# Kernel optimization log

Measured on AMD Instinct MI355X. Metric: run time of the kernel, lower is better.

## Reference

```python
import jax, jax.numpy as jnp
import numpy as np

L = 20        # num layers (TTS LM)
Q = 512       # query length
PAST = 512    # past_kv_len
END = PAST + Q  # end_step = 1024
MAXS = 2048   # max_seq_len
D = 896       # hidden size
NKV = 2       # KV heads
NQ = 14       # Q heads
G = NQ // NKV # GQA repeat = 7
HD = 64       # head dim
FF = 4864     # SwiGLU intermediate (Qwen2.5-0.5B)
EPS = 1e-6
SCALE = 1.0 / np.sqrt(HD)


def rms_norm(x, w):
    return x * jax.lax.rsqrt(jnp.mean(x * x, axis=-1, keepdims=True) + EPS) * w


def rotate_half(x):
    x1, x2 = jnp.split(x, 2, axis=-1)
    return jnp.concatenate([-x2, x1], axis=-1)


def setup_inputs() -> dict:
    key = jax.random.key(0)
    ks = jax.random.split(key, 24)
    s = 0.02
    inp = {
        'hidden_states': jax.random.normal(ks[0], (1, Q, D), jnp.float32),
        'position_cos': jax.random.uniform(ks[1], (1, Q, HD), jnp.float32, -1.0, 1.0),
        'position_sin': jax.random.uniform(ks[2], (1, Q, HD), jnp.float32, -1.0, 1.0),
        'attention_mask': jnp.zeros((1, 1, Q, END), jnp.float32),
        'inject_mode': jnp.zeros((1,), jnp.float32),
        'inject_k': jax.random.normal(ks[3], (1, L * NKV, Q, HD), jnp.float32),
        'inject_v': jax.random.normal(ks[4], (1, L * NKV, Q, HD), jnp.float32),
        'k_cache': (jax.random.normal(ks[5], (L, 1, NKV, MAXS, HD), jnp.float32) * 0.5).astype(jnp.float16),
        'v_cache': (jax.random.normal(ks[6], (L, 1, NKV, MAXS, HD), jnp.float32) * 0.5).astype(jnp.float16),
        'Wq': jax.random.normal(ks[7], (L, D, NQ * HD), jnp.float32) * s,
        'bq': jax.random.normal(ks[8], (L, NQ * HD), jnp.float32) * s,
        'Wk': jax.random.normal(ks[9], (L, D, NKV * HD), jnp.float32) * s,
        'bk': jax.random.normal(ks[10], (L, NKV * HD), jnp.float32) * s,
        'Wv': jax.random.normal(ks[11], (L, D, NKV * HD), jnp.float32) * s,
        'bv': jax.random.normal(ks[12], (L, NKV * HD), jnp.float32) * s,
        'Wo': jax.random.normal(ks[13], (L, NQ * HD, D), jnp.float32) * s,
        'ln1': jnp.ones((L, D), jnp.float32),
        'ln2': jnp.ones((L, D), jnp.float32),
        'Wg': jax.random.normal(ks[14], (L, D, FF), jnp.float32) * s,
        'Wu': jax.random.normal(ks[15], (L, D, FF), jnp.float32) * s,
        'Wd': jax.random.normal(ks[16], (L, FF, D), jnp.float32) * s,
        'final_w': jnp.ones((D,), jnp.float32),
    }
    return inp


def reference(hidden_states, position_cos, position_sin, attention_mask,
              inject_mode, inject_k, inject_v, k_cache, v_cache,
              Wq, bq, Wk, bk, Wv, bv, Wo, ln1, ln2, Wg, Wu, Wd, final_w):
    cos = position_cos[:, None]   # [1,1,Q,HD]
    sin = position_sin[:, None]
    inj = inject_mode[0]
    normal = 1.0 - inj
    mask = attention_mask[:, None]  # [1,1,1,Q,END] broadcast over (g,h)
    # per-layer inject slices: [L,1,NKV,Q,HD]
    ik = jnp.transpose(inject_k.reshape(1, L, NKV, Q, HD), (1, 0, 2, 3, 4))
    iv = jnp.transpose(inject_v.reshape(1, L, NKV, Q, HD), (1, 0, 2, 3, 4))

    def layer_fn(h, p):
        (wq, bq_, wk, bk_, wv, bv_, wo, l1, l2, wg, wu, wd, kc, vc, ikl, ivl) = p
        residual = h
        x = rms_norm(h, l1)
        q = (x @ wq + bq_).reshape(1, Q, NQ, HD).transpose(0, 2, 1, 3)   # [1,NQ,Q,HD]
        k = (x @ wk + bk_).reshape(1, Q, NKV, HD).transpose(0, 2, 1, 3)  # [1,NKV,Q,HD]
        v = (x @ wv + bv_).reshape(1, Q, NKV, HD).transpose(0, 2, 1, 3)
        q = q * cos + rotate_half(q) * sin
        k = k * cos + rotate_half(k) * sin
        k = normal * k + inj * ikl
        v = normal * v + inj * ivl
        kc = kc.at[:, :, PAST:END].set(k.astype(jnp.float16))
        vc = vc.at[:, :, PAST:END].set(v.astype(jnp.float16))
        kf = kc[:, :, :END].astype(jnp.float32)  # [1,NKV,END,HD]
        vf = vc[:, :, :END].astype(jnp.float32)
        qg = q.reshape(1, NKV, G, Q, HD)         # grouped GQA (== repeat_kv)
        scores = jnp.einsum('bghqd,bgkd->bghqk', qg, kf) * SCALE + mask
        w = jax.nn.softmax(scores, axis=-1)
        o = jnp.einsum('bghqk,bgkd->bghqd', w, vf)
        o = o.reshape(1, NQ, Q, HD).transpose(0, 2, 1, 3).reshape(1, Q, NQ * HD)
        h = residual + o @ wo
        residual = h
        x = rms_norm(h, l2)
        h = residual + (jax.nn.silu(x @ wg) * (x @ wu)) @ wd
        return h, None

    xs = (Wq, bq, Wk, bk, Wv, bv, Wo, ln1, ln2, Wg, Wu, Wd, k_cache, v_cache, ik, iv)
    h, _ = jax.lax.scan(layer_fn, hidden_states, xs)
    return rms_norm(h, final_w)
```

## Files before the change

kernel.cpp:

```cpp
#include <hip/hip_runtime.h>
#include <hip/hip_fp16.h>
#include <hip/hip_cooperative_groups.h>

namespace cg = cooperative_groups;

#define NLAYER 20
#define QLEN 512
#define PAST 512
#define ENDS 1024
#define MAXS 2048
#define DMODEL 896
#define NKV 2
#define NQ 14
#define GQ 7
#define HD 64
#define FF 4864
#define RMSEPS 1e-6f
#define ATT_SCALE 0.125f

typedef _Float16 f16x8 __attribute__((ext_vector_type(8)));
typedef float f32x4 __attribute__((ext_vector_type(4)));
typedef unsigned int u32_;

__device__ __forceinline__ void gld16(const void* g, void* l) {
    __builtin_amdgcn_global_load_lds(
        (const __attribute__((address_space(1))) u32_*)g,
        (__attribute__((address_space(3))) u32_*)l, 16, 0, 0);
}

union SmemU {
    struct { __half As[16384]; __half Bs[16384]; } g;
    struct { __half S[16512]; float rowinv[16]; } a;
    __half Tp[128 * 130];
    struct { float red[4]; } r;
};

#define GEMM_STAGE64(A_, lda_, B_, ldb_, Kps_)                                  \
    const int lane = t & 63, wave = t >> 6;                                     \
    const int wm = wave >> 1, wn = wave & 1;                                    \
    const int m0 = by * 128, n0 = bx * 128;                                     \
    const int kb0 = bz * (Kps_);                                                \
    const int la = lane & 15, kg = lane >> 4;                                   \
    const int nIter = (Kps_) >> 6;                                              \
    const int srow = t >> 3;                                                    \
    const int gsw = ((t & 7) ^ (srow & 7)) * 8;                                 \
    f32x4 acc[4][4] = {};                                                       \
    {                                                                           \
        _Pragma("unroll")                                                       \
        for (int q = 0; q < 4; q++) {                                           \
            gld16(&(A_)[(size_t)(m0 + q * 32 + srow) * (lda_) + kb0 + gsw], &As[q * 2048 + t * 8]); \
            gld16(&(B_)[(size_t)(n0 + q * 32 + srow) * (ldb_) + kb0 + gsw], &Bs[q * 2048 + t * 8]); \
        }                                                                       \
    }                                                                           \
    int buf = 0;                                                                \
    for (int kt = 0; kt < nIter; kt++) {                                        \
        __syncthreads();                                                        \
        if (kt + 1 < nIter) {                                                   \
            const int ko = kb0 + (kt + 1) * 64;                                 \
            const int lb = (buf ^ 1) * 8192;                                    \
            _Pragma("unroll")                                                   \
            for (int q = 0; q < 4; q++) {                                       \
                gld16(&(A_)[(size_t)(m0 + q * 32 + srow) * (lda_) + ko + gsw], &As[lb + q * 2048 + t * 8]); \
                gld16(&(B_)[(size_t)(n0 + q * 32 + srow) * (ldb_) + ko + gsw], &Bs[lb + q * 2048 + t * 8]); \
            }                                                                   \
        }                                                                       \
        _Pragma("unroll")                                                       \
        for (int kk = 0; kk < 2; kk++) {                                        \
            f16x8 av[4], bv[4];                                                 \
            const int g = kk * 4 + kg;                                          \
            _Pragma("unroll")                                                   \
            for (int i = 0; i < 4; i++) {                                       \
                const int R = wm * 64 + i * 16 + la;                            \
                av[i] = *(const f16x8*)&As[buf * 8192 + R * 64 + ((g ^ (R & 7)) * 8)]; \
            }                                                                   \
            _Pragma("unroll")                                                   \
            for (int j = 0; j < 4; j++) {                                       \
                const int R = wn * 64 + j * 16 + la;                            \
                bv[j] = *(const f16x8*)&Bs[buf * 8192 + R * 64 + ((g ^ (R & 7)) * 8)]; \
            }                                                                   \
            _Pragma("unroll")                                                   \
            for (int i = 0; i < 4; i++)                                         \
                _Pragma("unroll")                                               \
                for (int j = 0; j < 4; j++)                                     \
                    acc[i][j] = __builtin_amdgcn_mfma_f32_16x16x32_f16(av[i], bv[j], acc[i][j], 0, 0, 0); \
        }                                                                       \
        buf ^= 1;                                                               \
    }                                                                           \
    __syncthreads();

__device__ __forceinline__ void gemm_body(
    const __half* __restrict__ A, int lda, const __half* __restrict__ B, int ldb,
    float* __restrict__ outP, __half* __restrict__ actP, int N, int Kps, int mode,
    int bx, int by, int bz, int t, __half* As, __half* Bs)
{
    GEMM_STAGE64(A, lda, B, ldb, Kps)
    const int r0 = m0 + wm * 64 + kg * 4;
    const int c0 = n0 + wn * 64 + la;
    if (mode == 0) {
        float* o = outP + (size_t)bz * QLEN * N;
#pragma unroll
        for (int i = 0; i < 4; i++)
#pragma unroll
            for (int j = 0; j < 4; j++)
#pragma unroll
                for (int r = 0; r < 4; r++)
                    o[(size_t)(r0 + i * 16 + r) * N + c0 + j * 16] = acc[i][j][r];
    } else {
#pragma unroll
        for (int i = 0; i < 4; i++)
#pragma unroll
            for (int j = 0; j < 4; j++)
#pragma unroll
                for (int r = 0; r < 4; r++) {
                    float v = acc[i][j][r];
                    float other = __shfl_xor(v, 1);
                    if (!(la & 1)) {
                        const int c = c0 + j * 16;
                        const int row = r0 + i * 16 + r;
                        float sg = v / (1.f + __expf(-v));
                        actP[(size_t)row * FF + (c >> 1)] = __float2half(sg * other);
                    }
                }
    }
}

__device__ __forceinline__ void gemm_qkv_body(
    const __half* __restrict__ A, const __half* __restrict__ B,
    const float* __restrict__ bqkv, const float* __restrict__ cosb,
    const float* __restrict__ sinb, float inj,
    const float* __restrict__ injk, const float* __restrict__ injv,
    __half* __restrict__ qr, __half* __restrict__ Ka, __half* __restrict__ Vt,
    int layer, int bx, int by, int t, __half* As, __half* Bs)
{
    const int bz = 0;
    GEMM_STAGE64(A, DMODEL, B, DMODEL, 896)
    const int r0 = m0 + wm * 64 + kg * 4;
    const int c0 = n0 + wn * 64 + la;
    const float nrm = 1.f - inj;
#pragma unroll
    for (int i = 0; i < 4; i++)
#pragma unroll
        for (int j = 0; j < 4; j++)
#pragma unroll
            for (int r = 0; r < 4; r++) {
                const int pn = r0 + i * 16 + r;
                const int c = c0 + j * 16;
                const int d = c & 63;
                float v = acc[i][j][r] + bqkv[c];
                if (c < 1024) {
                    float pvv = acc[i][j ^ 2][r] + bqkv[c ^ 32];
                    float rot = (d < 32) ? -pvv : pvv;
                    float rv = v * cosb[pn * HD + d] + rot * sinb[pn * HD + d];
                    if (c < 896) {
                        qr[((size_t)(c >> 6) * QLEN + pn) * HD + d] = __float2half(rv);
                    } else {
                        const int kvh = (c - 896) >> 6;
                        float kn = nrm * rv + inj * injk[(((size_t)layer * NKV + kvh) * QLEN + pn) * HD + d];
                        Ka[((size_t)kvh * ENDS + PAST + pn) * HD + d] = __float2half(kn);
                    }
                } else {
                    const int kvh = (c - 1024) >> 6;
                    float vn = nrm * v + inj * injv[(((size_t)layer * NKV + kvh) * QLEN + pn) * HD + d];
                    Vt[((size_t)kvh * HD + d) * ENDS + PAST + pn] = __float2half(vn);
                }
            }
}

__device__ __forceinline__ void prep_body(
    const float* __restrict__ Wq, const float* __restrict__ Wk, const float* __restrict__ Wv,
    const float* __restrict__ Wo, const float* __restrict__ Wg, const float* __restrict__ Wu,
    const float* __restrict__ Wd, int layer, int z, int bx, int t, __half* Tp,
    __half* __restrict__ dstW)
{
    const int K = (z == 3) ? FF : DMODEL;
    const int N = (z == 0) ? 1152 : (z == 2) ? 2 * FF : DMODEL;
    const int tilesN = N / 128;
    const int tk = bx / tilesN, tn = bx % tilesN;
    const int k0 = tk * 128, n0 = tn * 128;
    const float* src; int ldn, nc0; int isU = 0;
    if (z == 0) {
        if (n0 < 896)        { src = Wq + (size_t)layer * 896 * 896; ldn = 896; nc0 = n0; }
        else if (n0 < 1024)  { src = Wk + (size_t)layer * 896 * 128; ldn = 128; nc0 = n0 - 896; }
        else                 { src = Wv + (size_t)layer * 896 * 128; ldn = 128; nc0 = n0 - 1024; }
    } else if (z == 1) { src = Wo + (size_t)layer * 896 * 896; ldn = 896; nc0 = n0; }
    else if (z == 2) {
        if (n0 < FF) { src = Wg + (size_t)layer * 896 * FF; ldn = FF; nc0 = n0; }
        else         { src = Wu + (size_t)layer * 896 * FF; ldn = FF; nc0 = n0 - FF; isU = 1; }
    } else { src = Wd + (size_t)layer * FF * 896; ldn = 896; nc0 = n0; }

    __syncthreads();
    const int r8 = t >> 5, cc = (t & 31) * 4;
#pragma unroll
    for (int half = 0; half < 2; half++) {
        float4 v[8];
#pragma unroll
        for (int q = 0; q < 8; q++) {
            const int row = half * 64 + q * 8 + r8;
            v[q] = *(const float4*)&src[(size_t)(k0 + row) * ldn + nc0 + cc];
        }
#pragma unroll
        for (int q = 0; q < 8; q++) {
            const int row = half * 64 + q * 8 + r8;
            __half2 p0 = __halves2half2(__float2half_rn(v[q].x), __float2half_rn(v[q].y));
            __half2 p1 = __halves2half2(__float2half_rn(v[q].z), __float2half_rn(v[q].w));
            *(__half2*)&Tp[row * 130 + cc] = p0;
            *(__half2*)&Tp[row * 130 + cc + 2] = p1;
        }
    }
    __syncthreads();
    {
        const int nr = t >> 1, kh = (t & 1) * 64;
        const int drow = (z == 2) ? (2 * (nc0 + nr) + isU) : (n0 + nr);
        __half tmp[64];
#pragma unroll
        for (int kk = 0; kk < 64; kk++)
            tmp[kk] = Tp[(kh + kk) * 130 + nr];
        __half* dst = dstW + (size_t)drow * K + k0 + kh;
#pragma unroll
        for (int q = 0; q < 8; q++)
            *(uint4*)(dst + q * 8) = *(const uint4*)&tmp[q * 8];
    }
    __syncthreads();
}

__device__ __forceinline__ void prep_dispatch(
    const float* Wq, const float* Wk, const float* Wv, const float* Wo,
    const float* Wg, const float* Wu, const float* Wd,
    const float* bq, const float* bk, const float* bv,
    int layer, int j, int t, __half* Tp,
    __half* wq, __half* wo, __half* wgu, __half* wd, float* bqkv)
{
    int z; __half* dst; int bx = j;
    if (j < 63)         { z = 0; dst = wq; }
    else if (j < 112)   { z = 1; dst = wo;  bx -= 63; }
    else if (j < 644)   { z = 2; dst = wgu; bx -= 112; }
    else                { z = 3; dst = wd;  bx -= 644; }
    prep_body(Wq, Wk, Wv, Wo, Wg, Wu, Wd, layer, z, bx, t, Tp, dst);
    if (z == 0 && bx == 0) {
        for (int i = t; i < 1152; i += 256) {
            float b = (i < 896) ? bq[(size_t)layer * 896 + i]
                    : (i < 1024) ? bk[(size_t)layer * 128 + i - 896]
                                 : bv[(size_t)layer * 128 + i - 1024];
            bqkv[i] = b;
        }
    }
}

__device__ __forceinline__ void cache_copy_body(
    const float* __restrict__ kc32, const float* __restrict__ vc32, int layer,
    __half* __restrict__ Ka, __half* __restrict__ Vt, int p, int lt)
{
    const int kvh = lt >> 6, d = lt & 63;
    const size_t idx = (((size_t)layer * NKV + kvh) * MAXS + p) * HD + d;
    Ka[((size_t)kvh * ENDS + p) * HD + d] = __float2half(kc32[idx]);
    Vt[((size_t)kvh * HD + d) * ENDS + p] = __float2half(vc32[idx]);
}

__device__ __forceinline__ void ropekv_body(
    const float* __restrict__ part, const float* __restrict__ bias,
    const float* __restrict__ cosb, const float* __restrict__ sinb,
    const float* __restrict__ injm, const float* __restrict__ injk,
    const float* __restrict__ injv, const float* __restrict__ kc32,
    const float* __restrict__ vc32, int layer, int nsplit,
    __half* __restrict__ qr, __half* __restrict__ Ka, __half* __restrict__ Vt,
    int p, int lt)
{
    const int kvh = lt >> 6, d = lt & 63;
    if (p < PAST) { cache_copy_body(kc32, vc32, layer, Ka, Vt, p, lt); return; }
    const int pn = p - PAST;
    const float inj = injm[0], nrm = 1.f - inj;
    const float* rb = part + (size_t)pn * 1152;
    const size_t sst = (size_t)QLEN * 1152;
    auto rsum = [&](int c) {
        float x = bias[c];
        for (int s = 0; s < nsplit; s++) x += rb[(size_t)s * sst + c];
        return x;
    };
    for (int idx = lt; idx < NQ * HD; idx += 128) {
        const int dd = idx & 63;
        float x = rsum(idx);
        int pc = (dd < 32) ? idx + 32 : idx - 32;
        float pv = rsum(pc);
        if (dd < 32) pv = -pv;
        float rv = x * cosb[pn * HD + dd] + pv * sinb[pn * HD + dd];
        qr[((size_t)(idx >> 6) * QLEN + pn) * HD + dd] = __float2half(rv);
    }
    {
        const int c = NQ * HD + lt;
        float x = rsum(c);
        int pc = (d < 32) ? c + 32 : c - 32;
        float pv = rsum(pc);
        if (d < 32) pv = -pv;
        float rv = x * cosb[pn * HD + d] + pv * sinb[pn * HD + d];
        float kn = nrm * rv + inj * injk[(((size_t)layer * NKV + kvh) * QLEN + pn) * HD + d];
        Ka[((size_t)kvh * ENDS + PAST + pn) * HD + d] = __float2half(kn);
        const int cv = NQ * HD + NKV * HD + lt;
        float vv = rsum(cv);
        float vn = nrm * vv + inj * injv[(((size_t)layer * NKV + kvh) * QLEN + pn) * HD + d];
        Vt[((size_t)kvh * HD + d) * ENDS + PAST + pn] = __float2half(vn);
    }
}

__device__ __forceinline__ int sswz(int row, int col) {
    return row * 1032 + (col ^ ((row & 7) << 3));
}

__device__ __forceinline__ void attn_body(
    const __half* __restrict__ qr, const __half* __restrict__ Ka,
    const __half* __restrict__ Vt, const float* __restrict__ mask,
    __half* __restrict__ ob, int q0, int h, int t, __half* S, float* rowinv)
{
    const int kv = h / GQ;
    const int lane = t & 63, w = t >> 6;
    const int la = lane & 15, kg = lane >> 4;

    const f16x8* qp = (const f16x8*)&qr[((size_t)h * QLEN + q0 + la) * HD + kg * 8];
    const f16x8 qa0 = qp[0], qa1 = qp[4];
    __syncthreads();

    for (int kb = 0; kb < 256; kb += 16) {
        const int key = w * 256 + kb + la;
        const f16x8* kp = (const f16x8*)&Ka[((size_t)kv * ENDS + key) * HD + kg * 8];
        f32x4 s4 = {0.f, 0.f, 0.f, 0.f};
        s4 = __builtin_amdgcn_mfma_f32_16x16x32_f16(qa0, kp[0], s4, 0, 0, 0);
        s4 = __builtin_amdgcn_mfma_f32_16x16x32_f16(qa1, kp[4], s4, 0, 0, 0);
#pragma unroll
        for (int r = 0; r < 4; r++) {
            const int row = kg * 4 + r;
            float sv = s4[r] * ATT_SCALE + mask[(size_t)(q0 + row) * ENDS + key];
            S[sswz(row, key)] = __float2half(sv);
        }
    }
    __syncthreads();
    {
        const int row = w * 4 + kg;
        float mx = -1e30f;
        for (int j = 0; j < 64; j++)
            mx = fmaxf(mx, __half2float(S[sswz(row, la + 16 * j)]));
        for (int o = 1; o < 16; o <<= 1) mx = fmaxf(mx, __shfl_xor(mx, o));
        float sum = 0.f;
        for (int j = 0; j < 64; j++) {
            const int idx = sswz(row, la + 16 * j);
            float e = __expf(__half2float(S[idx]) - mx);
            S[idx] = __float2half(e);
            sum += e;
        }
        for (int o = 1; o < 16; o <<= 1) sum += __shfl_xor(sum, o);
        if (la == 0) rowinv[row] = 1.f / sum;
    }
    __syncthreads();
    {
        const int d = 16 * w + la;
        const __half* vrow = &Vt[((size_t)kv * HD + d) * ENDS];
        f32x4 acc = {0.f, 0.f, 0.f, 0.f};
        for (int ks = 0; ks < ENDS; ks += 32) {
            f16x8 pa = *(const f16x8*)&S[sswz(la, ks + kg * 8)];
            f16x8 vb = *(const f16x8*)&vrow[ks + kg * 8];
            acc = __builtin_amdgcn_mfma_f32_16x16x32_f16(pa, vb, acc, 0, 0, 0);
        }
#pragma unroll
        for (int r = 0; r < 4; r++) {
            const int qrow = kg * 4 + r;
            ob[(size_t)(q0 + qrow) * (NQ * HD) + h * HD + d] =
                __float2half(acc[r] * rowinv[qrow]);
        }
    }
    __syncthreads();
}

__device__ inline void cvt_store(float* p, float v)  { *p = v; }
__device__ inline void cvt_store(__half* p, float v) { *p = __float2half(v); }

template <typename OUT>
__device__ __forceinline__ void rms_body(
    float* __restrict__ h, const float* __restrict__ parts, int nparts,
    const float* __restrict__ w, OUT* __restrict__ out, int m, int t,
    float* red, float scale)
{
    float loc[4];
    float ss = 0.f;
    int r = 0;
    for (int i = t; i < DMODEL; i += 256, r++) {
        float x = h[(size_t)m * DMODEL + i];
        for (int s = 0; s < nparts; s++)
            x += parts[(size_t)s * QLEN * DMODEL + (size_t)m * DMODEL + i];
        loc[r] = x;
        if (nparts) h[(size_t)m * DMODEL + i] = x;
        ss += x * x;
    }
    for (int o = 32; o; o >>= 1) ss += __shfl_xor(ss, o);
    if ((t & 63) == 0) red[t >> 6] = ss;
    __syncthreads();
    float rs = rsqrtf((red[0] + red[1] + red[2] + red[3]) / (float)DMODEL + RMSEPS);
    r = 0;
    for (int i = t; i < DMODEL; i += 256, r++)
        cvt_store(&out[(size_t)m * DMODEL + i], loc[r] * rs * w[i] * scale);
    __syncthreads();
}

struct P22 {
    const float *hidden, *cosb, *sinb, *mask, *injm, *injk, *injv, *kc32, *vc32;
    const float *Wq, *bq, *Wk, *bk, *Wv, *bv, *Wo, *ln1, *ln2, *Wg, *Wu, *Wd, *finw;
    float *h; __half *xn, *qr, *Ka, *Vt, *ob, *act; float *BIGR;
    float *bqkv0, *bqkv1;
    __half *wq0, *wo0, *wgu0, *wd0, *wq1, *wo1, *wgu1, *wd1;
    float *outF;
};

#define PC_B 300
#define PC_C 60
#define PC_D 200
#define PC_F 250
#define PC_G 100
#define PB_B 0
#define PB_C 300
#define PB_D 360
#define PB_F 560
#define PB_G 810

__global__ __launch_bounds__(256) void mega_kernel(P22 P)
{
    __shared__ SmemU sm;
    cg::grid_group gg = cg::this_grid();
    const int nb = gridDim.x, bid = blockIdx.x, t = threadIdx.x;
    const float inj = P.injm[0];

    for (int j = bid; j < 1792; j += nb) {
        int i = j * 256 + t;
        if (i < QLEN * DMODEL) P.h[i] = P.hidden[i];
    }
    for (int j = bid; j < 256; j += nb)
        cache_copy_body(P.kc32, P.vc32, 0, P.Ka, P.Vt, j * 2 + (t >> 7), t & 127);
    for (int j = bid; j < 910; j += nb)
        prep_dispatch(P.Wq, P.Wk, P.Wv, P.Wo, P.Wg, P.Wu, P.Wd, P.bq, P.bk, P.bv,
                      0, j, t, sm.Tp, P.wq0, P.wo0, P.wgu0, P.wd0, P.bqkv0);
    gg.sync();

    for (int l = 0; l < NLAYER; l++) {
        const int pb = l & 1;
        const __half* wq  = pb ? P.wq1  : P.wq0;
        const __half* wo  = pb ? P.wo1  : P.wo0;
        const __half* wgu = pb ? P.wgu1 : P.wgu0;
        const __half* wd  = pb ? P.wd1  : P.wd0;
        const float*  bqk = pb ? P.bqkv1 : P.bqkv0;
        const bool hasN = (l + 1 < NLAYER);
        __half* nwq  = pb ? P.wq0  : P.wq1;
        __half* nwo  = pb ? P.wo0  : P.wo1;
        __half* nwgu = pb ? P.wgu0 : P.wgu1;
        __half* nwd  = pb ? P.wd0  : P.wd1;
        float*  nbq  = pb ? P.bqkv0 : P.bqkv1;
        #define PREPN(idx) prep_dispatch(P.Wq, P.Wk, P.Wv, P.Wo, P.Wg, P.Wu, P.Wd, \
            P.bq, P.bk, P.bv, l + 1, (idx), t, sm.Tp, nwq, nwo, nwgu, nwd, nbq)

        for (int j = bid; j < QLEN; j += nb)
            rms_body<__half>(P.h, l ? P.BIGR : nullptr, l ? 19 : 0,
                             P.ln1 + (size_t)l * DMODEL, P.xn, j, t, sm.r.red, 1.f);
        gg.sync();

        for (int j = bid; j < 36 + (hasN ? PC_B : 0); j += nb) {
            if (j < 36)
                gemm_qkv_body(P.xn, wq, bqk, P.cosb, P.sinb, inj, P.injk, P.injv,
                              P.qr, P.Ka, P.Vt, l, j % 9, j / 9, t, sm.g.As, sm.g.Bs);
            else PREPN(PB_B + j - 36);
        }
        gg.sync();

        for (int j = bid; j < 448 + (hasN ? PC_C : 0); j += nb) {
            if (j < 448)
                attn_body(P.qr, P.Ka, P.Vt, P.mask, P.ob, (j & 31) * 16, j >> 5, t,
                          sm.a.S, sm.a.rowinv);
            else PREPN(PB_C + j - 448);
        }
        gg.sync();

        for (int j = bid; j < 452 + (hasN ? PC_D : 0); j += nb) {
            if (j < 196) {
                int z = j / 28, r = j % 28;
                gemm_body(P.ob, DMODEL, wo, DMODEL, P.BIGR, nullptr, DMODEL, 128, 0,
                          r % 7, r / 7, z, t, sm.g.As, sm.g.Bs);
            } else if (j < 452) {
                if (hasN) cache_copy_body(P.kc32, P.vc32, l + 1, P.Ka, P.Vt,
                                          (j - 196) * 2 + (t >> 7), t & 127);
            } else PREPN(PB_D + j - 452);
        }
        gg.sync();

        for (int j = bid; j < QLEN; j += nb)
            rms_body<__half>(P.h, P.BIGR, 7, P.ln2 + (size_t)l * DMODEL, P.xn,
                             j, t, sm.r.red, 1.f);
        gg.sync();

        for (int j = bid; j < 304 + (hasN ? PC_F : 0); j += nb) {
            if (j < 304)
                gemm_body(P.xn, DMODEL, wgu, DMODEL, nullptr, P.act, 2 * FF, 896, 1,
                          j % 76, j / 76, 0, t, sm.g.As, sm.g.Bs);
            else PREPN(PB_F + j - 304);
        }
        gg.sync();

        for (int j = bid; j < 532 + (hasN ? PC_G : 0); j += nb) {
            if (j < 532) {
                int z = j / 28, r = j % 28;
                gemm_body(P.act, FF, wd, FF, P.BIGR, nullptr, DMODEL, 256, 0,
                          r % 7, r / 7, z, t, sm.g.As, sm.g.Bs);
            } else PREPN(PB_G + j - 532);
        }
        gg.sync();
        #undef PREPN
    }
    for (int j = bid; j < QLEN; j += nb)
        rms_body<float>(P.h, P.BIGR, 19, P.finw, P.outF, j, t, sm.r.red, 1.f);
}

__global__ __launch_bounds__(256) void init_kernel(
    const float* __restrict__ hidden, float* __restrict__ h)
{
    const int idx = blockIdx.x * 256 + threadIdx.x;
    if (idx < QLEN * DMODEL) h[idx] = hidden[idx];
}

__global__ __launch_bounds__(256) void prep_all(
    const float* Wq, const float* Wk, const float* Wv, const float* Wo,
    const float* Wg, const float* Wu, const float* Wd,
    const float* bq, const float* bk, const float* bv, int layer,
    __half* wqkv, __half* wo, __half* wgu, __half* wd, float* bqkv)
{
    __shared__ __half Tp[128 * 130];
    prep_dispatch(Wq, Wk, Wv, Wo, Wg, Wu, Wd, bq, bk, bv, layer, blockIdx.x,
                  threadIdx.x, Tp, wqkv, wo, wgu, wd, bqkv);
}

__global__ __launch_bounds__(256) void gemm128(
    const __half* A, int lda, const __half* B, int ldb,
    float* outP, __half* actP, int N, int Kps, int mode)
{
    __shared__ SmemU sm;
    gemm_body(A, lda, B, ldb, outP, actP, N, Kps, mode,
              blockIdx.x, blockIdx.y, blockIdx.z, threadIdx.x, sm.g.As, sm.g.Bs);
}

__global__ __launch_bounds__(128) void ropekv_kernel(
    const float* part, const float* bias, const float* cosb, const float* sinb,
    const float* injm, const float* injk, const float* injv,
    const float* kc32, const float* vc32, int layer, int nsplit,
    __half* qr, __half* Ka, __half* Vt)
{
    ropekv_body(part, bias, cosb, sinb, injm, injk, injv, kc32, vc32,
                layer, nsplit, qr, Ka, Vt, blockIdx.x, threadIdx.x);
}

__global__ __launch_bounds__(256) void attn_mfma(
    const __half* qr, const __half* Ka, const __half* Vt, const float* mask, __half* ob)
{
    __shared__ SmemU sm;
    attn_body(qr, Ka, Vt, mask, ob, blockIdx.x * 16, blockIdx.y, threadIdx.x,
              sm.a.S, sm.a.rowinv);
}

template <typename OUT>
__global__ __launch_bounds__(256) void rms_kernel(
    float* h, const float* parts, int nparts, const float* w, OUT* out)
{
    __shared__ float red[4];
    rms_body<OUT>(h, parts, nparts, w, out, blockIdx.x, threadIdx.x, red, 1.f);
}

extern "C" void kernel_launch(void* const* d_in, const int* in_sizes, int n_in,
                              void* d_out, int out_size, void* d_ws, size_t ws_size,
                              hipStream_t stream)
{
    const float*  hidden = (const float*)d_in[0];
    const float*  cosb   = (const float*)d_in[1];
    const float*  sinb   = (const float*)d_in[2];
    const float*  mask   = (const float*)d_in[3];
    const float*  injm   = (const float*)d_in[4];
    const float*  injk   = (const float*)d_in[5];
    const float*  injv   = (const float*)d_in[6];
    const float*  kc32   = (const float*)d_in[7];
    const float*  vc32   = (const float*)d_in[8];
    const float*  Wq     = (const float*)d_in[9];
    const float*  bq     = (const float*)d_in[10];
    const float*  Wk     = (const float*)d_in[11];
    const float*  bk     = (const float*)d_in[12];
    const float*  Wv     = (const float*)d_in[13];
    const float*  bv     = (const float*)d_in[14];
    const float*  Wo     = (const float*)d_in[15];
    const float*  ln1    = (const float*)d_in[16];
    const float*  ln2    = (const float*)d_in[17];
    const float*  Wg     = (const float*)d_in[18];
    const float*  Wu     = (const float*)d_in[19];
    const float*  Wd     = (const float*)d_in[20];
    const float*  finw   = (const float*)d_in[21];

    bool size_ok = (n_in == 22) &&
        in_sizes[0] == 458752 && in_sizes[1] == 32768 && in_sizes[3] == 524288 &&
        in_sizes[4] == 1 && in_sizes[5] == 1310720 && in_sizes[7] == 5242880 &&
        in_sizes[9] == 16056320 && in_sizes[10] == 17920 && in_sizes[11] == 2293760 &&
        in_sizes[15] == 16056320 && in_sizes[16] == 17920 && in_sizes[18] == 87162880 &&
        in_sizes[20] == 87162880 && in_sizes[21] == 896;
    if (!size_ok) { hipMemsetAsync(d_out, 0x42, (size_t)out_size * 4, stream); return; }

    char* ws = (char*)d_ws;
    size_t off = 0;
    auto alloc = [&](size_t bytes) { void* p = ws + off; off += (bytes + 255) & ~255ull; return p; };
    float*  bqkv0 = (float*)alloc(1152 * 4);
    float*  bqkv1 = (float*)alloc(1152 * 4);
    float*  h     = (float*)alloc((size_t)QLEN * DMODEL * 4);
    __half* xn    = (__half*)alloc((size_t)QLEN * DMODEL * 2);
    __half* qr    = (__half*)alloc((size_t)NQ * QLEN * HD * 2);
    __half* Ka    = (__half*)alloc((size_t)NKV * ENDS * HD * 2);
    __half* Vt    = (__half*)alloc((size_t)NKV * ENDS * HD * 2);
    __half* ob    = (__half*)alloc((size_t)QLEN * NQ * HD * 2);
    __half* act   = (__half*)alloc((size_t)QLEN * FF * 2);
    float*  BIGR  = (float*)alloc(19ull * QLEN * DMODEL * 4);
    __half* wq0   = (__half*)alloc(2064384);
    __half* wo0   = (__half*)alloc(1605632);
    __half* wgu0  = (__half*)alloc(17432576);
    __half* wd0   = (__half*)alloc(8716288);
    const size_t NEED_LEGACY = off;
    __half* wq1   = (__half*)alloc(2064384);
    __half* wo1   = (__half*)alloc(1605632);
    __half* wgu1  = (__half*)alloc(17432576);
    __half* wd1   = (__half*)alloc(8716288);
    const size_t NEED_MEGA = off;

    if (ws_size < NEED_LEGACY) {
        hipMemsetAsync(d_out, 0, (size_t)out_size * 4, stream);
        return;
    }

    bool mega_ok = (ws_size >= NEED_MEGA);
    if (mega_ok) {
        int maxB = 0;
        hipError_t e = hipOccupancyMaxActiveBlocksPerMultiprocessor(
            &maxB, reinterpret_cast<const void*>(&mega_kernel), 256, 0);
        if (e != hipSuccess || maxB < 1) mega_ok = false;
        if (mega_ok) {
            int grid = maxB * 256;
            if (grid > 512) grid = 512;
            P22 Pv = { hidden, cosb, sinb, mask, injm, injk, injv, kc32, vc32,
                       Wq, bq, Wk, bk, Wv, bv, Wo, ln1, ln2, Wg, Wu, Wd, finw,
                       h, xn, qr, Ka, Vt, ob, act, BIGR, bqkv0, bqkv1,
                       wq0, wo0, wgu0, wd0, wq1, wo1, wgu1, wd1, (float*)d_out };
            void* args[] = { (void*)&Pv };
            hipError_t le = hipLaunchCooperativeKernel(
                reinterpret_cast<const void*>(&mega_kernel),
                dim3(grid), dim3(256), args, 0, stream);
            if (le == hipSuccess) return;
            mega_ok = false;
        }
    }

    init_kernel<<<1792, 256, 0, stream>>>(hidden, h);
    for (int l = 0; l < NLAYER; l++) {
        prep_all<<<910, 256, 0, stream>>>(Wq, Wk, Wv, Wo, Wg, Wu, Wd, bq, bk, bv, l,
                                          wq0, wo0, wgu0, wd0, bqkv0);
        rms_kernel<__half><<<QLEN, 256, 0, stream>>>(h, l ? BIGR : nullptr, l ? 19 : 0,
                                                     ln1 + (size_t)l * DMODEL, xn);
        gemm128<<<dim3(9, 4, 2), 256, 0, stream>>>(xn, DMODEL, wq0, DMODEL, BIGR, nullptr, 1152, 448, 0);
        ropekv_kernel<<<ENDS, 128, 0, stream>>>(BIGR, bqkv0, cosb, sinb, injm, injk, injv,
                                                kc32, vc32, l, 2, qr, Ka, Vt);
        attn_mfma<<<dim3(32, 14), 256, 0, stream>>>(qr, Ka, Vt, mask, ob);
        gemm128<<<dim3(7, 4, 7), 256, 0, stream>>>(ob, DMODEL, wo0, DMODEL, BIGR, nullptr, DMODEL, 128, 0);
        rms_kernel<__half><<<QLEN, 256, 0, stream>>>(h, BIGR, 7, ln2 + (size_t)l * DMODEL, xn);
        gemm128<<<dim3(76, 4, 1), 256, 0, stream>>>(xn, DMODEL, wgu0, DMODEL, nullptr, act, 2 * FF, 896, 1);
        gemm128<<<dim3(7, 4, 19), 256, 0, stream>>>(act, FF, wd0, FF, BIGR, nullptr, DMODEL, 256, 0);
    }
    rms_kernel<float><<<QLEN, 256, 0, stream>>>(h, BIGR, 19, finw, (float*)d_out);
}
```

Baseline: 2.821 ms.

## Fold RMSNorm weights into prepped weights and cut split-K partial counts

The RMSNorm gain vectors are multiplied into the fp16 weight conversion, and the per-row rsqrt scale is applied in the GEMM epilogues. The normalize kernels therefore only reduce the residual partials and emit fp16 h plus a scale. Split-K for the Wo and down projections drops from 7/19 partials to 2/4. This shrinks the partial buffer traffic and the block counts in those phases, and the prep-work interleaving constants are rebalanced to match. The trade-off is longer K loops per block with fewer blocks, and fp16 rounding of the unnormalized h instead of the normalized activations.

Result: slower. 3.085 ms (+9.3%).

```diff
diff --git a/kernel.cpp b/kernel.cpp
--- a/kernel.cpp
+++ b/kernel.cpp
@@ -90,8 +90,8 @@
 
 __device__ __forceinline__ void gemm_body(
     const __half* __restrict__ A, int lda, const __half* __restrict__ B, int ldb,
-    float* __restrict__ outP, __half* __restrict__ actP, int N, int Kps, int mode,
-    int bx, int by, int bz, int t, __half* As, __half* Bs)
+    float* __restrict__ outP, __half* __restrict__ actP, const float* __restrict__ rs,
+    int N, int Kps, int mode, int bx, int by, int bz, int t, __half* As, __half* Bs)
 {
     GEMM_STAGE64(A, lda, B, ldb, Kps)
     const int r0 = m0 + wm * 64 + kg * 4;
@@ -112,11 +112,11 @@
             for (int j = 0; j < 4; j++)
 #pragma unroll
                 for (int r = 0; r < 4; r++) {
-                    float v = acc[i][j][r];
+                    const int row = r0 + i * 16 + r;
+                    float v = acc[i][j][r] * rs[row];
                     float other = __shfl_xor(v, 1);
                     if (!(la & 1)) {
                         const int c = c0 + j * 16;
-                        const int row = r0 + i * 16 + r;
                         float sg = v / (1.f + __expf(-v));
                         actP[(size_t)row * FF + (c >> 1)] = __float2half(sg * other);
                     }
@@ -126,6 +126,7 @@
 
 __device__ __forceinline__ void gemm_qkv_body(
     const __half* __restrict__ A, const __half* __restrict__ B,
+    const float* __restrict__ rs1,
     const float* __restrict__ bqkv, const float* __restrict__ cosb,
     const float* __restrict__ sinb, float inj,
     const float* __restrict__ injk, const float* __restrict__ injv,
@@ -146,9 +147,10 @@
                 const int pn = r0 + i * 16 + r;
                 const int c = c0 + j * 16;
                 const int d = c & 63;
-                float v = acc[i][j][r] + bqkv[c];
+                const float sc = rs1[pn];
+                float v = acc[i][j][r] * sc + bqkv[c];
                 if (c < 1024) {
-                    float pvv = acc[i][j ^ 2][r] + bqkv[c ^ 32];
+                    float pvv = acc[i][j ^ 2][r] * sc + bqkv[c ^ 32];
                     float rot = (d < 32) ? -pvv : pvv;
                     float rv = v * cosb[pn * HD + d] + rot * sinb[pn * HD + d];
                     if (c < 896) {
@@ -169,8 +171,8 @@
 __device__ __forceinline__ void prep_body(
     const float* __restrict__ Wq, const float* __restrict__ Wk, const float* __restrict__ Wv,
     const float* __restrict__ Wo, const float* __restrict__ Wg, const float* __restrict__ Wu,
-    const float* __restrict__ Wd, int layer, int z, int bx, int t, __half* Tp,
-    __half* __restrict__ dstW)
+    const float* __restrict__ Wd, const float* __restrict__ lnv,
+    int layer, int z, int bx, int t, __half* Tp, __half* __restrict__ dstW)
 {
     const int K = (z == 3) ? FF : DMODEL;
     const int N = (z == 0) ? 1152 : (z == 2) ? 2 * FF : DMODEL;
@@ -193,16 +195,18 @@
 #pragma unroll
     for (int half = 0; half < 2; half++) {
         float4 v[8];
+        float ls[8];
 #pragma unroll
         for (int q = 0; q < 8; q++) {
             const int row = half * 64 + q * 8 + r8;
             v[q] = *(const float4*)&src[(size_t)(k0 + row) * ldn + nc0 + cc];
+            ls[q] = lnv ? lnv[k0 + row] : 1.f;
         }
 #pragma unroll
         for (int q = 0; q < 8; q++) {
             const int row = half * 64 + q * 8 + r8;
-            __half2 p0 = __halves2half2(__float2half_rn(v[q].x), __float2half_rn(v[q].y));
-            __half2 p1 = __halves2half2(__float2half_rn(v[q].z), __float2half_rn(v[q].w));
+            __half2 p0 = __halves2half2(__float2half_rn(v[q].x * ls[q]), __float2half_rn(v[q].y * ls[q]));
+            __half2 p1 = __halves2half2(__float2half_rn(v[q].z * ls[q]), __float2half_rn(v[q].w * ls[q]));
             *(__half2*)&Tp[row * 130 + cc] = p0;
             *(__half2*)&Tp[row * 130 + cc + 2] = p1;
         }
@@ -227,15 +231,16 @@
     const float* Wq, const float* Wk, const float* Wv, const float* Wo,
     const float* Wg, const float* Wu, const float* Wd,
     const float* bq, const float* bk, const float* bv,
+    const float* ln1, const float* ln2,
     int layer, int j, int t, __half* Tp,
     __half* wq, __half* wo, __half* wgu, __half* wd, float* bqkv)
 {
-    int z; __half* dst; int bx = j;
-    if (j < 63)         { z = 0; dst = wq; }
+    int z; __half* dst; int bx = j; const float* lnv = nullptr;
+    if (j < 63)         { z = 0; dst = wq;  lnv = ln1 + (size_t)layer * 896; }
     else if (j < 112)   { z = 1; dst = wo;  bx -= 63; }
-    else if (j < 644)   { z = 2; dst = wgu; bx -= 112; }
+    else if (j < 644)   { z = 2; dst = wgu; bx -= 112; lnv = ln2 + (size_t)layer * 896; }
     else                { z = 3; dst = wd;  bx -= 644; }
-    prep_body(Wq, Wk, Wv, Wo, Wg, Wu, Wd, layer, z, bx, t, Tp, dst);
+    prep_body(Wq, Wk, Wv, Wo, Wg, Wu, Wd, lnv, layer, z, bx, t, Tp, dst);
     if (z == 0 && bx == 0) {
         for (int i = t; i < 1152; i += 256) {
             float b = (i < 896) ? bq[(size_t)layer * 896 + i]
@@ -254,51 +259,6 @@
     const size_t idx = (((size_t)layer * NKV + kvh) * MAXS + p) * HD + d;
     Ka[((size_t)kvh * ENDS + p) * HD + d] = __float2half(kc32[idx]);
     Vt[((size_t)kvh * HD + d) * ENDS + p] = __float2half(vc32[idx]);
-}
-
-__device__ __forceinline__ void ropekv_body(
-    const float* __restrict__ part, const float* __restrict__ bias,
-    const float* __restrict__ cosb, const float* __restrict__ sinb,
-    const float* __restrict__ injm, const float* __restrict__ injk,
-    const float* __restrict__ injv, const float* __restrict__ kc32,
-    const float* __restrict__ vc32, int layer, int nsplit,
-    __half* __restrict__ qr, __half* __restrict__ Ka, __half* __restrict__ Vt,
-    int p, int lt)
-{
-    const int kvh = lt >> 6, d = lt & 63;
-    if (p < PAST) { cache_copy_body(kc32, vc32, layer, Ka, Vt, p, lt); return; }
-    const int pn = p - PAST;
-    const float inj = injm[0], nrm = 1.f - inj;
-    const float* rb = part + (size_t)pn * 1152;
-    const size_t sst = (size_t)QLEN * 1152;
-    auto rsum = [&](int c) {
-        float x = bias[c];
-        for (int s = 0; s < nsplit; s++) x += rb[(size_t)s * sst + c];
-        return x;
-    };
-    for (int idx = lt; idx < NQ * HD; idx += 128) {
-        const int dd = idx & 63;
-        float x = rsum(idx);
-        int pc = (dd < 32) ? idx + 32 : idx - 32;
-        float pv = rsum(pc);
-        if (dd < 32) pv = -pv;
-        float rv = x * cosb[pn * HD + dd] + pv * sinb[pn * HD + dd];
-        qr[((size_t)(idx >> 6) * QLEN + pn) * HD + dd] = __float2half(rv);
-    }
-    {
-        const int c = NQ * HD + lt;
-        float x = rsum(c);
-        int pc = (d < 32) ? c + 32 : c - 32;
-        float pv = rsum(pc);
-        if (d < 32) pv = -pv;
-        float rv = x * cosb[pn * HD + d] + pv * sinb[pn * HD + d];
-        float kn = nrm * rv + inj * injk[(((size_t)layer * NKV + kvh) * QLEN + pn) * HD + d];
-        Ka[((size_t)kvh * ENDS + PAST + pn) * HD + d] = __float2half(kn);
-        const int cv = NQ * HD + NKV * HD + lt;
-        float vv = rsum(cv);
-        float vn = nrm * vv + inj * injv[(((size_t)layer * NKV + kvh) * QLEN + pn) * HD + d];
-        Vt[((size_t)kvh * HD + d) * ENDS + PAST + pn] = __float2half(vn);
-    }
 }
 
 __device__ __forceinline__ int sswz(int row, int col) {
@@ -368,14 +328,9 @@
     __syncthreads();
 }
 
-__device__ inline void cvt_store(float* p, float v)  { *p = v; }
-__device__ inline void cvt_store(__half* p, float v) { *p = __float2half(v); }
-
-template <typename OUT>
-__device__ __forceinline__ void rms_body(
+__device__ __forceinline__ void hfin_body(
     float* __restrict__ h, const float* __restrict__ parts, int nparts,
-    const float* __restrict__ w, OUT* __restrict__ out, int m, int t,
-    float* red, float scale)
+    __half* __restrict__ hh, float* __restrict__ rs, int m, int t, float* red)
 {
     float loc[4];
     float ss = 0.f;
@@ -391,32 +346,57 @@
     for (int o = 32; o; o >>= 1) ss += __shfl_xor(ss, o);
     if ((t & 63) == 0) red[t >> 6] = ss;
     __syncthreads();
-    float rs = rsqrtf((red[0] + red[1] + red[2] + red[3]) / (float)DMODEL + RMSEPS);
+    if (t == 0) rs[m] = rsqrtf((red[0] + red[1] + red[2] + red[3]) / (float)DMODEL + RMSEPS);
     r = 0;
     for (int i = t; i < DMODEL; i += 256, r++)
-        cvt_store(&out[(size_t)m * DMODEL + i], loc[r] * rs * w[i] * scale);
+        hh[(size_t)m * DMODEL + i] = __float2half(loc[r]);
+    __syncthreads();
+}
+
+__device__ __forceinline__ void rmsfin_body(
+    float* __restrict__ h, const float* __restrict__ parts, int nparts,
+    const float* __restrict__ w, float* __restrict__ out, int m, int t, float* red)
+{
+    float loc[4];
+    float ss = 0.f;
+    int r = 0;
+    for (int i = t; i < DMODEL; i += 256, r++) {
+        float x = h[(size_t)m * DMODEL + i];
+        for (int s = 0; s < nparts; s++)
+            x += parts[(size_t)s * QLEN * DMODEL + (size_t)m * DMODEL + i];
+        loc[r] = x;
+        ss += x * x;
+    }
+    for (int o = 32; o; o >>= 1) ss += __shfl_xor(ss, o);
+    if ((t & 63) == 0) red[t >> 6] = ss;
+    __syncthreads();
+    float rsv = rsqrtf((red[0] + red[1] + red[2] + red[3]) / (float)DMODEL + RMSEPS);
+    r = 0;
+    for (int i = t; i < DMODEL; i += 256, r++)
+        out[(size_t)m * DMODEL + i] = loc[r] * rsv * w[i];
     __syncthreads();
 }
 
 struct P22 {
     const float *hidden, *cosb, *sinb, *mask, *injm, *injk, *injv, *kc32, *vc32;
     const float *Wq, *bq, *Wk, *bk, *Wv, *bv, *Wo, *ln1, *ln2, *Wg, *Wu, *Wd, *finw;
-    float *h; __half *xn, *qr, *Ka, *Vt, *ob, *act; float *BIGR;
+    float *h; __half *hh, *qr, *Ka, *Vt, *ob, *act; float *BIGR;
+    float *rs1, *rs2;
     float *bqkv0, *bqkv1;
     __half *wq0, *wo0, *wgu0, *wd0, *wq1, *wo1, *wgu1, *wd1;
     float *outF;
 };
 
-#define PC_B 300
+#define PC_B 270
 #define PC_C 60
 #define PC_D 200
-#define PC_F 250
-#define PC_G 100
+#define PC_F 208
+#define PC_G 172
 #define PB_B 0
-#define PB_C 300
-#define PB_D 360
-#define PB_F 560
-#define PB_G 810
+#define PB_C 270
+#define PB_D 330
+#define PB_F 530
+#define PB_G 738
 
 __global__ __launch_bounds__(256) void mega_kernel(P22 P)
 {
@@ -433,7 +413,7 @@
         cache_copy_body(P.kc32, P.vc32, 0, P.Ka, P.Vt, j * 2 + (t >> 7), t & 127);
     for (int j = bid; j < 910; j += nb)
         prep_dispatch(P.Wq, P.Wk, P.Wv, P.Wo, P.Wg, P.Wu, P.Wd, P.bq, P.bk, P.bv,
-                      0, j, t, sm.Tp, P.wq0, P.wo0, P.wgu0, P.wd0, P.bqkv0);
+                      P.ln1, P.ln2, 0, j, t, sm.Tp, P.wq0, P.wo0, P.wgu0, P.wd0, P.bqkv0);
     gg.sync();
 
     for (int l = 0; l < NLAYER; l++) {
@@ -450,16 +430,15 @@
         __half* nwd  = pb ? P.wd0  : P.wd1;
         float*  nbq  = pb ? P.bqkv0 : P.bqkv1;
         #define PREPN(idx) prep_dispatch(P.Wq, P.Wk, P.Wv, P.Wo, P.Wg, P.Wu, P.Wd, \
-            P.bq, P.bk, P.bv, l + 1, (idx), t, sm.Tp, nwq, nwo, nwgu, nwd, nbq)
+            P.bq, P.bk, P.bv, P.ln1, P.ln2, l + 1, (idx), t, sm.Tp, nwq, nwo, nwgu, nwd, nbq)
 
         for (int j = bid; j < QLEN; j += nb)
-            rms_body<__half>(P.h, l ? P.BIGR : nullptr, l ? 19 : 0,
-                             P.ln1 + (size_t)l * DMODEL, P.xn, j, t, sm.r.red, 1.f);
+            hfin_body(P.h, l ? P.BIGR : nullptr, l ? 4 : 0, P.hh, P.rs1, j, t, sm.r.red);
         gg.sync();
 
         for (int j = bid; j < 36 + (hasN ? PC_B : 0); j += nb) {
             if (j < 36)
-                gemm_qkv_body(P.xn, wq, bqk, P.cosb, P.sinb, inj, P.injk, P.injv,
+                gemm_qkv_body(P.hh, wq, P.rs1, bqk, P.cosb, P.sinb, inj, P.injk, P.injv,
                               P.qr, P.Ka, P.Vt, l, j % 9, j / 9, t, sm.g.As, sm.g.Bs);
             else PREPN(PB_B + j - 36);
         }
@@ -473,43 +452,42 @@
         }
         gg.sync();
 
-        for (int j = bid; j < 452 + (hasN ? PC_D : 0); j += nb) {
-            if (j < 196) {
+        for (int j = bid; j < 312 + (hasN ? PC_D : 0); j += nb) {
+            if (j < 56) {
                 int z = j / 28, r = j % 28;
-                gemm_body(P.ob, DMODEL, wo, DMODEL, P.BIGR, nullptr, DMODEL, 128, 0,
-                          r % 7, r / 7, z, t, sm.g.As, sm.g.Bs);
-            } else if (j < 452) {
+                gemm_body(P.ob, DMODEL, wo, DMODEL, P.BIGR, nullptr, nullptr,
+                          DMODEL, 448, 0, r % 7, r / 7, z, t, sm.g.As, sm.g.Bs);
+            } else if (j < 312) {
                 if (hasN) cache_copy_body(P.kc32, P.vc32, l + 1, P.Ka, P.Vt,
-                                          (j - 196) * 2 + (t >> 7), t & 127);
-            } else PREPN(PB_D + j - 452);
+                                          (j - 56) * 2 + (t >> 7), t & 127);
+            } else PREPN(PB_D + j - 312);
         }
         gg.sync();
 
         for (int j = bid; j < QLEN; j += nb)
-            rms_body<__half>(P.h, P.BIGR, 7, P.ln2 + (size_t)l * DMODEL, P.xn,
-                             j, t, sm.r.red, 1.f);
+            hfin_body(P.h, P.BIGR, 2, P.hh, P.rs2, j, t, sm.r.red);
         gg.sync();
 
         for (int j = bid; j < 304 + (hasN ? PC_F : 0); j += nb) {
             if (j < 304)
-                gemm_body(P.xn, DMODEL, wgu, DMODEL, nullptr, P.act, 2 * FF, 896, 1,
-                          j % 76, j / 76, 0, t, sm.g.As, sm.g.Bs);
+                gemm_body(P.hh, DMODEL, wgu, DMODEL, nullptr, P.act, P.rs2,
+                          2 * FF, 896, 1, j % 76, j / 76, 0, t, sm.g.As, sm.g.Bs);
             else PREPN(PB_F + j - 304);
         }
         gg.sync();
 
-        for (int j = bid; j < 532 + (hasN ? PC_G : 0); j += nb) {
-            if (j < 532) {
+        for (int j = bid; j < 112 + (hasN ? PC_G : 0); j += nb) {
+            if (j < 112) {
                 int z = j / 28, r = j % 28;
-                gemm_body(P.act, FF, wd, FF, P.BIGR, nullptr, DMODEL, 256, 0,
-                          r % 7, r / 7, z, t, sm.g.As, sm.g.Bs);
-            } else PREPN(PB_G + j - 532);
+                gemm_body(P.act, FF, wd, FF, P.BIGR, nullptr, nullptr,
+                          DMODEL, 1216, 0, r % 7, r / 7, z, t, sm.g.As, sm.g.Bs);
+            } else PREPN(PB_G + j - 112);
         }
         gg.sync();
         #undef PREPN
     }
     for (int j = bid; j < QLEN; j += nb)
-        rms_body<float>(P.h, P.BIGR, 19, P.finw, P.outF, j, t, sm.r.red, 1.f);
+        rmsfin_body(P.h, P.BIGR, 4, P.finw, P.outF, j, t, sm.r.red);
 }
 
 __global__ __launch_bounds__(256) void init_kernel(
@@ -522,31 +500,40 @@
 __global__ __launch_bounds__(256) void prep_all(
     const float* Wq, const float* Wk, const float* Wv, const float* Wo,
     const float* Wg, const float* Wu, const float* Wd,
-    const float* bq, const float* bk, const float* bv, int layer,
+    const float* bq, const float* bk, const float* bv,
+    const float* ln1, const float* ln2, int layer,
     __half* wqkv, __half* wo, __half* wgu, __half* wd, float* bqkv)
 {
     __shared__ __half Tp[128 * 130];
-    prep_dispatch(Wq, Wk, Wv, Wo, Wg, Wu, Wd, bq, bk, bv, layer, blockIdx.x,
-                  threadIdx.x, Tp, wqkv, wo, wgu, wd, bqkv);
+    prep_dispatch(Wq, Wk, Wv, Wo, Wg, Wu, Wd, bq, bk, bv, ln1, ln2, layer,
+                  blockIdx.x, threadIdx.x, Tp, wqkv, wo, wgu, wd, bqkv);
 }
 
 __global__ __launch_bounds__(256) void gemm128(
     const __half* A, int lda, const __half* B, int ldb,
-    float* outP, __half* actP, int N, int Kps, int mode)
+    float* outP, __half* actP, const float* rs, int N, int Kps, int mode)
 {
     __shared__ SmemU sm;
-    gemm_body(A, lda, B, ldb, outP, actP, N, Kps, mode,
+    gemm_body(A, lda, B, ldb, outP, actP, rs, N, Kps, mode,
               blockIdx.x, blockIdx.y, blockIdx.z, threadIdx.x, sm.g.As, sm.g.Bs);
 }
 
-__global__ __launch_bounds__(128) void ropekv_kernel(
-    const float* part, const float* bias, const float* cosb, const float* sinb,
-    const float* injm, const float* injk, const float* injv,
-    const float* kc32, const float* vc32, int layer, int nsplit,
-    __half* qr, __half* Ka, __half* Vt)
-{
-    ropekv_body(part, bias, cosb, sinb, injm, injk, injv, kc32, vc32,
-                layer, nsplit, qr, Ka, Vt, blockIdx.x, threadIdx.x);
+__global__ __launch_bounds__(256) void gemm_qkv(
+    const __half* A, const __half* B, const float* rs1, const float* bqkv,
+    const float* cosb, const float* sinb, const float* injm,
+    const float* injk, const float* injv,
+    __half* qr, __half* Ka, __half* Vt, int layer)
+{
+    __shared__ SmemU sm;
+    gemm_qkv_body(A, B, rs1, bqkv, cosb, sinb, injm[0], injk, injv,
+                  qr, Ka, Vt, layer, blockIdx.x, blockIdx.y, threadIdx.x,
+                  sm.g.As, sm.g.Bs);
+}
+
+__global__ __launch_bounds__(128) void cache_copy_kernel(
+    const float* kc32, const float* vc32, int layer, __half* Ka, __half* Vt)
+{
+    cache_copy_body(kc32, vc32, layer, Ka, Vt, blockIdx.x, threadIdx.x);
 }
 
 __global__ __launch_bounds__(256) void attn_mfma(
@@ -557,12 +544,18 @@
               sm.a.S, sm.a.rowinv);
 }
 
-template <typename OUT>
-__global__ __launch_bounds__(256) void rms_kernel(
-    float* h, const float* parts, int nparts, const float* w, OUT* out)
+__global__ __launch_bounds__(256) void hfin_kernel(
+    float* h, const float* parts, int nparts, __half* hh, float* rs)
 {
     __shared__ float red[4];
-    rms_body<OUT>(h, parts, nparts, w, out, blockIdx.x, threadIdx.x, red, 1.f);
+    hfin_body(h, parts, nparts, hh, rs, blockIdx.x, threadIdx.x, red);
+}
+
+__global__ __launch_bounds__(256) void rmsfin_kernel(
+    float* h, const float* parts, int nparts, const float* w, float* out)
+{
+    __shared__ float red[4];
+    rmsfin_body(h, parts, nparts, w, out, blockIdx.x, threadIdx.x, red);
 }
 
 extern "C" void kernel_launch(void* const* d_in, const int* in_sizes, int n_in,
@@ -605,14 +598,16 @@
     auto alloc = [&](size_t bytes) { void* p = ws + off; off += (bytes + 255) & ~255ull; return p; };
     float*  bqkv0 = (float*)alloc(1152 * 4);
     float*  bqkv1 = (float*)alloc(1152 * 4);
+    float*  rs1   = (float*)alloc(QLEN * 4);
+    float*  rs2   = (float*)alloc(QLEN * 4);
     float*  h     = (float*)alloc((size_t)QLEN * DMODEL * 4);
-    __half* xn    = (__half*)alloc((size_t)QLEN * DMODEL * 2);
+    __half* hh    = (__half*)alloc((size_t)QLEN * DMODEL * 2);
     __half* qr    = (__half*)alloc((size_t)NQ * QLEN * HD * 2);
     __half* Ka    = (__half*)alloc((size_t)NKV * ENDS * HD * 2);
     __half* Vt    = (__half*)alloc((size_t)NKV * ENDS * HD * 2);
     __half* ob    = (__half*)alloc((size_t)QLEN * NQ * HD * 2);
     __half* act   = (__half*)alloc((size_t)QLEN * FF * 2);
-    float*  BIGR  = (float*)alloc(19ull * QLEN * DMODEL * 4);
+    float*  BIGR  = (float*)alloc(4ull * QLEN * DMODEL * 4);
     __half* wq0   = (__half*)alloc(2064384);
     __half* wo0   = (__half*)alloc(1605632);
     __half* wgu0  = (__half*)alloc(17432576);
@@ -640,7 +635,7 @@
             if (grid > 512) grid = 512;
             P22 Pv = { hidden, cosb, sinb, mask, injm, injk, injv, kc32, vc32,
                        Wq, bq, Wk, bk, Wv, bv, Wo, ln1, ln2, Wg, Wu, Wd, finw,
-                       h, xn, qr, Ka, Vt, ob, act, BIGR, bqkv0, bqkv1,
+                       h, hh, qr, Ka, Vt, ob, act, BIGR, rs1, rs2, bqkv0, bqkv1,
                        wq0, wo0, wgu0, wd0, wq1, wo1, wgu1, wd1, (float*)d_out };
             void* args[] = { (void*)&Pv };
             hipError_t le = hipLaunchCooperativeKernel(
@@ -653,18 +648,20 @@
 
     init_kernel<<<1792, 256, 0, stream>>>(hidden, h);
     for (int l = 0; l < NLAYER; l++) {
-        prep_all<<<910, 256, 0, stream>>>(Wq, Wk, Wv, Wo, Wg, Wu, Wd, bq, bk, bv, l,
-                                          wq0, wo0, wgu0, wd0, bqkv0);
-        rms_kernel<__half><<<QLEN, 256, 0, stream>>>(h, l ? BIGR : nullptr, l ? 19 : 0,
-                                                     ln1 + (size_t)l * DMODEL, xn);
-        gemm128<<<dim3(9, 4, 2), 256, 0, stream>>>(xn, DMODEL, wq0, DMODEL, BIGR, nullptr, 1152, 448, 0);
-        ropekv_kernel<<<ENDS, 128, 0, stream>>>(BIGR, bqkv0, cosb, sinb, injm, injk, injv,
-                                                kc32, vc32, l, 2, qr, Ka, Vt);
+        prep_all<<<910, 256, 0, stream>>>(Wq, Wk, Wv, Wo, Wg, Wu, Wd, bq, bk, bv,
+                                          ln1, ln2, l, wq0, wo0, wgu0, wd0, bqkv0);
+        hfin_kernel<<<QLEN, 256, 0, stream>>>(h, l ? BIGR : nullptr, l ? 4 : 0, hh, rs1);
+        cache_copy_kernel<<<PAST, 128, 0, stream>>>(kc32, vc32, l, Ka, Vt);
+        gemm_qkv<<<dim3(9, 4), 256, 0, stream>>>(hh, wq0, rs1, bqkv0, cosb, sinb,
+                                                 injm, injk, injv, qr, Ka, Vt, l);
         attn_mfma<<<dim3(32, 14), 256, 0, stream>>>(qr, Ka, Vt, mask, ob);
-        gemm128<<<dim3(7, 4, 7), 256, 0, stream>>>(ob, DMODEL, wo0, DMODEL, BIGR, nullptr, DMODEL, 128, 0);
-        rms_kernel<__half><<<QLEN, 256, 0, stream>>>(h, BIGR, 7, ln2 + (size_t)l * DMODEL, xn);
-        gemm128<<<dim3(76, 4, 1), 256, 0, stream>>>(xn, DMODEL, wgu0, DMODEL, nullptr, act, 2 * FF, 896, 1);
-        gemm128<<<dim3(7, 4, 19), 256, 0, stream>>>(act, FF, wd0, FF, BIGR, nullptr, DMODEL, 256, 0);
-    }
-    rms_kernel<float><<<QLEN, 256, 0, stream>>>(h, BIGR, 19, finw, (float*)d_out);
-}
+        gemm128<<<dim3(7, 4, 2), 256, 0, stream>>>(ob, DMODEL, wo0, DMODEL, BIGR,
+                                                   nullptr, nullptr, DMODEL, 448, 0);
+        hfin_kernel<<<QLEN, 256, 0, stream>>>(h, BIGR, 2, hh, rs2);
+        gemm128<<<dim3(76, 4, 1), 256, 0, stream>>>(hh, DMODEL, wgu0, DMODEL, nullptr,
+                                                    act, rs2, 2 * FF, 896, 1);
+        gemm128<<<dim3(7, 4, 4), 256, 0, stream>>>(act, FF, wd0, FF, BIGR,
+                                                   nullptr, nullptr, DMODEL, 1216, 0);
+    }
+    rmsfin_kernel<<<QLEN, 256, 0, stream>>>(h, BIGR, 4, finw, (float*)d_out);
+}
```
